# Performance work log

Measured on AMD Instinct MI355X. Metric: run time of the kernel, lower is better.

The kernel has to match this reference:

```python
import jax, jax.numpy as jnp
import numpy as np

N_U = 50000
N_I = 50000
E = 800000
E_LBL = 200000
D_IN = 128
HID = 256
OUT = 128


def setup_inputs() -> dict:
    key = jax.random.key(0)
    ks = jax.random.split(key, 32)
    def glorot(k, shp):
        fan = shp[0] + shp[1]
        return jax.random.uniform(k, shp, jnp.float32, -1.0, 1.0) * np.sqrt(6.0 / fan)
    inp = {
        'x_user': jax.random.normal(ks[0], (N_U, D_IN), jnp.float32),
        'x_item': jax.random.normal(ks[1], (N_I, D_IN), jnp.float32),
        'edge_ui': jax.random.randint(ks[2], (2, E), 0, N_U, jnp.int32),
        'edge_iu': jax.random.randint(ks[3], (2, E), 0, N_I, jnp.int32),
        'edge_lbl': jax.random.randint(ks[4], (2, E_LBL), 0, N_U, jnp.int32),
        # layer 0 SAGE params (src_dim=D_IN, dst_dim=D_IN)
        'w_msg_ui0': glorot(ks[5], (D_IN, HID)), 'b_ui0': jnp.zeros((HID,), jnp.float32), 'w_root_ui0': glorot(ks[6], (D_IN, HID)),
        'w_msg_iu0': glorot(ks[7], (D_IN, HID)), 'b_iu0': jnp.zeros((HID,), jnp.float32), 'w_root_iu0': glorot(ks[8], (D_IN, HID)),
        # layer 1 SAGE params (src_dim=HID, dst_dim=HID)
        'w_msg_ui1': glorot(ks[9], (HID, HID)), 'b_ui1': jnp.zeros((HID,), jnp.float32), 'w_root_ui1': glorot(ks[10], (HID, HID)),
        'w_msg_iu1': glorot(ks[11], (HID, HID)), 'b_iu1': jnp.zeros((HID,), jnp.float32), 'w_root_iu1': glorot(ks[12], (HID, HID)),
        # per-node-type output linears on JK concat (2*HID -> OUT)
        'w_lin_u': glorot(ks[13], (2 * HID, OUT)), 'b_lin_u': jnp.zeros((OUT,), jnp.float32),
        'w_lin_i': glorot(ks[14], (2 * HID, OUT)), 'b_lin_i': jnp.zeros((OUT,), jnp.float32),
    }
    return inp


def _sage(x_src, x_dst, edge, w_msg, b_msg, w_root):
    # PyG SAGEConv(aggr='mean'): lin_l(mean_{j in N(i)} x_src[j]) + lin_r(x_dst[i])
    src, dst = edge[0], edge[1]
    n_dst = x_dst.shape[0]
    agg = jax.ops.segment_sum(x_src[src], dst, num_segments=n_dst)          # [n_dst, d_src]
    cnt = jax.ops.segment_sum(jnp.ones((edge.shape[1],), x_src.dtype), dst, num_segments=n_dst)
    mean = agg / jnp.maximum(cnt, 1.0)[:, None]
    return mean @ w_msg + b_msg + x_dst @ w_root


def reference(x_user, x_item, edge_ui, edge_iu, edge_lbl,
              w_msg_ui0, b_ui0, w_root_ui0, w_msg_iu0, b_iu0, w_root_iu0,
              w_msg_ui1, b_ui1, w_root_ui1, w_msg_iu1, b_iu1, w_root_iu1,
              w_lin_u, b_lin_u, w_lin_i, b_lin_i):
    # ----- encode: 2 HeteroConv(SAGEConv) layers -----
    item0 = _sage(x_user, x_item, edge_ui, w_msg_ui0, b_ui0, w_root_ui0)    # user->item
    user0 = _sage(x_item, x_user, edge_iu, b_msg=b_iu0, w_msg=w_msg_iu0, x_src=None, x_dst=None, edge=None, w_root=None) if False else _sage(x_item, x_user, edge_iu, w_msg_iu0, b_iu0, w_root_iu0)  # item->user
    item1 = _sage(user0, item0, edge_ui, w_msg_ui1, b_ui1, w_root_ui1)
    user1 = _sage(item0, user0, edge_iu, w_msg_iu1, b_iu1, w_root_iu1)
    # ----- JumpingKnowledge 'cat' + per-node-type linear -----
    z_user = jnp.concatenate([user0, user1], axis=-1) @ w_lin_u + b_lin_u   # [N_U, OUT]
    z_item = jnp.concatenate([item0, item1], axis=-1) @ w_lin_i + b_lin_i   # [N_I, OUT]
    # ----- decode: dot product over candidate edges (user, buys, item) -----
    pred = jnp.sum(z_user[edge_lbl[0]] * z_item[edge_lbl[1]], axis=-1)      # [E_LBL]
    return pred
```

## Files before the change

### kernel.cpp

```cpp
#include <hip/hip_runtime.h>

#define NU 50000
#define NI 50000
#define NE 800000
#define NLBL 200000
#define DIN 128
#define HID 256
#define DOUT 128

#define NSLICE 128
#define SLICE_SZ 6250
#define HALF_N 25000

typedef unsigned short ushort_t;
typedef __attribute__((ext_vector_type(8))) short bf16x8;
typedef __attribute__((ext_vector_type(4))) float f32x4;

__device__ __forceinline__ float bf2f(unsigned int u_shifted) {
    union { unsigned int i; float f; } v;
    v.i = u_shifted;
    return v.f;
}
__device__ __forceinline__ float bf_lo(unsigned int u) { return bf2f(u << 16); }
__device__ __forceinline__ float bf_hi(unsigned int u) { return bf2f(u & 0xffff0000u); }
__device__ __forceinline__ ushort_t f2bf(float f) {
    union { float f; unsigned int i; } v;
    v.f = f;
    unsigned int r = (v.i + 0x7FFFu + ((v.i >> 16) & 1u)) >> 16;
    return (ushort_t)r;
}
__device__ __forceinline__ void load_lds16(const ushort_t* g, ushort_t* s) {
    __builtin_amdgcn_global_load_lds(
        (const __attribute__((address_space(1))) void*)g,
        (__attribute__((address_space(3))) void*)s, 16, 0, 0);
}

#define CVT_PER 782
#define CVT_B (2 * CVT_PER)
#define SA_B 512
#define HIST_B (2 * NSLICE * 2)

struct P1Args {
    const int *eui, *eiu;
    ushort_t* cnt_s;
    const float *wm_ui1, *wr_ui1, *wm_iu1, *wr_iu1, *lin_i, *lin_u;
    float *G_i, *S_i, *G_u, *S_u;
    int* scan_part;
    const float* xu; ushort_t* xbu; const float* xi; ushort_t* xbi;
};

__global__ __launch_bounds__(256) void phase1(P1Args a) {
    __shared__ unsigned int cnt[HALF_N / 2];
    int b = blockIdx.x, t = threadIdx.x;
    if (b < HIST_B) {
        int g = b >> 8, s = (b >> 1) & 127, half = b & 1;
        for (int i = t; i < HALF_N / 2; i += 256) cnt[i] = 0;
        __syncthreads();
        const int* dst = (g ? a.eiu : a.eui) + NE;
        int hbase = half * HALF_N;
        int e0 = s * SLICE_SZ;
        for (int i = e0 + t; i < e0 + SLICE_SZ; i += 256) {
            int d = dst[i] - hbase;
            if ((unsigned)d < (unsigned)HALF_N)
                atomicAdd(&cnt[d >> 1], 1u << ((d & 1) * 16));
        }
        __syncthreads();
        unsigned int* outp = (unsigned int*)(a.cnt_s + ((size_t)(g * NSLICE + s)) * 50000 + hbase);
        for (int i = t; i < HALF_N / 2; i += 256) outp[i] = cnt[i];
    } else if (b < HIST_B + SA_B) {
        int r2 = b - HIST_B;
        int which = r2 >> 7;
        int e = (r2 & 127) * 256 + t;
        int k = e >> 7, n = e & 127;
        const float* W = (which == 0) ? a.wm_ui1 : (which == 1) ? a.wr_ui1
                       : (which == 2) ? a.wm_iu1 : a.wr_iu1;
        const float* L = (which < 2) ? a.lin_i : a.lin_u;
        float* O = (which == 0) ? a.G_i : (which == 1) ? a.S_i
                 : (which == 2) ? a.G_u : a.S_u;
        float s = (which & 1) ? L[k * 128 + n] : 0.f;
#pragma unroll 4
        for (int j = 0; j < HID; ++j) s += W[k * HID + j] * L[(HID + j) * 128 + n];
        O[k * 128 + n] = s;
    } else if (b == HIST_B + SA_B) {
        if (t < 64) a.scan_part[t] = 0;
    } else {
        int cb = b - (HIST_B + SA_B + 1);
        int which = (cb >= CVT_PER);
        if (which) cb -= CVT_PER;
        const float4* in = (const float4*)(which ? a.xi : a.xu);
        uint2* outp = (uint2*)(which ? a.xbi : a.xbu);
        const int n4 = NU * DIN / 4;
#pragma unroll
        for (int k = 0; k < 8; ++k) {
            int i = cb * 2048 + k * 256 + t;
            if (i < n4) {
                float4 v = in[i];
                uint2 o;
                o.x = (unsigned int)f2bf(v.x) | ((unsigned int)f2bf(v.y) << 16);
                o.y = (unsigned int)f2bf(v.z) | ((unsigned int)f2bf(v.w) << 16);
                outp[i] = o;
            }
        }
    }
}

struct SscanP2Args {
    ushort_t* cnt_s;
    int* totals;
    int* scan_part;
    const float *wm_ui0, *wr_ui0, *wm_iu0, *wr_iu0;
    const float *G_i, *S_i, *G_u, *S_u;
    const float *b_ui0, *b_iu0, *b_ui1, *b_iu1, *lin_i, *lin_u, *bl_i, *bl_u;
    ushort_t *VT1_i, *VT2_i, *VT3_i, *VT1_u, *VT2_u, *VT3_u;
    float *bz_i, *bz_u;
};

__global__ __launch_bounds__(256) void sscan_prep2(SscanP2Args a) {
    __shared__ int wsum[4];
    int b = blockIdx.x, t = threadIdx.x;
    if (b < 392) {
        if (b == 0 && t == 0) a.totals[100000] = 2 * NE;
        int idx = b * 256 + t;
        int run = 0;
        if (idx < 100000) {
            int g = idx / 50000, node = idx - g * 50000;
            size_t base = (size_t)g * NSLICE * 50000 + node;
#pragma unroll 4
            for (int s = 0; s < NSLICE; ++s) {
                size_t o = base + (size_t)s * 50000;
                int c = a.cnt_s[o];
                a.cnt_s[o] = (ushort_t)run;
                run += c;
            }
            a.totals[idx] = run;
        }
        int s = run;
#pragma unroll
        for (int off = 32; off > 0; off >>= 1) s += __shfl_down(s, off, 64);
        if ((t & 63) == 0) wsum[t >> 6] = s;
        __syncthreads();
        if (t == 0) atomicAdd(&a.scan_part[b >> 3], wsum[0] + wsum[1] + wsum[2] + wsum[3]);
    } else {
        int task = b - 392;
        if (task < 384) {
            int v = task >> 6;
            int e = (task & 63) * 256 + t;
            int k = e >> 7, n = e & 127;
            const float *A1, *X1, *A2 = nullptr, *X2 = nullptr;
            ushort_t* O;
            switch (v) {
                case 0: A1 = a.wm_ui0; X1 = a.S_i; A2 = a.wr_iu0; X2 = a.G_i; O = a.VT1_i; break;
                case 1: A1 = a.wr_ui0; X1 = a.S_i; O = a.VT2_i; break;
                case 2: A1 = a.wm_iu0; X1 = a.G_i; O = a.VT3_i; break;
                case 3: A1 = a.wm_iu0; X1 = a.S_u; A2 = a.wr_ui0; X2 = a.G_u; O = a.VT1_u; break;
                case 4: A1 = a.wr_iu0; X1 = a.S_u; O = a.VT2_u; break;
                default: A1 = a.wm_ui0; X1 = a.G_u; O = a.VT3_u; break;
            }
            float s = 0.f;
#pragma unroll 4
            for (int j = 0; j < HID; ++j) s += A1[k * HID + j] * X1[j * 128 + n];
            if (A2) {
#pragma unroll 4
                for (int j = 0; j < HID; ++j) s += A2[k * HID + j] * X2[j * 128 + n];
            }
            O[n * 128 + k] = f2bf(s);
        } else if (t < 128) {
            int user = task - 384;
            int n = t;
            const float* S = user ? a.S_u : a.S_i;
            const float* G = user ? a.G_u : a.G_i;
            const float* b_own0 = user ? a.b_iu0 : a.b_ui0;
            const float* b_oth0 = user ? a.b_ui0 : a.b_iu0;
            const float* b_own1 = user ? a.b_iu1 : a.b_ui1;
            const float* lin = user ? a.lin_u : a.lin_i;
            const float* bl = user ? a.bl_u : a.bl_i;
            float* o = user ? a.bz_u : a.bz_i;
            float s = bl[n];
            for (int j = 0; j < HID; ++j)
                s += b_own0[j] * S[j * 128 + n] + b_oth0[j] * G[j * 128 + n] +
                     b_own1[j] * lin[(HID + j) * 128 + n];
            o[n] = s;
        }
    }
}

__global__ __launch_bounds__(256) void scan3(int* __restrict__ d, const int* __restrict__ part,
                                             int n, int nb) {
    __shared__ int wsum[4];
    __shared__ int blockoff_sh;
    int b = blockIdx.x, t = threadIdx.x;
    int lane = t & 63, wv = t >> 6;
    if (t < 64) {
        int v = (t < nb) ? part[t] : 0;
        int incl = v;
#pragma unroll
        for (int off = 1; off < 64; off <<= 1) {
            int tv = __shfl_up(incl, off, 64);
            if (t >= off) incl += tv;
        }
        if (t == b) blockoff_sh = incl - v;
    }
    int i0 = b * 2048 + t * 8;
    int v[8];
    int tsum = 0;
#pragma unroll
    for (int k = 0; k < 8; ++k) {
        v[k] = (i0 + k < n) ? d[i0 + k] : 0;
        tsum += v[k];
    }
    int incl = tsum;
#pragma unroll
    for (int off = 1; off < 64; off <<= 1) {
        int tv = __shfl_up(incl, off, 64);
        if (lane >= off) incl += tv;
    }
    if (lane == 63) wsum[wv] = incl;
    __syncthreads();
    int woff = 0;
    for (int w = 0; w < wv; ++w) woff += wsum[w];
    int run = blockoff_sh + woff + (incl - tsum);
#pragma unroll
    for (int k = 0; k < 8; ++k) {
        if (i0 + k < n) d[i0 + k] = run;
        run += v[k];
    }
}

__global__ __launch_bounds__(256) void fill_lds(const int* __restrict__ eui,
                                                const int* __restrict__ eiu,
                                                const ushort_t* __restrict__ cnt_s,
                                                const int* __restrict__ rowstart,
                                                ushort_t* __restrict__ csr) {
    __shared__ unsigned int off[HALF_N / 2];
    int b = blockIdx.x, t = threadIdx.x;
    int g = b >> 8, s = (b >> 1) & 127, half = b & 1;
    const unsigned int* st =
        (const unsigned int*)(cnt_s + ((size_t)(g * NSLICE + s)) * 50000 + half * HALF_N);
    for (int i = t; i < HALF_N / 2; i += 256) off[i] = st[i];
    __syncthreads();
    const int* src = g ? eiu : eui;
    const int* dst = src + NE;
    const int* rs = rowstart + g * 50000;
    int hbase = half * HALF_N;
    int e0 = s * SLICE_SZ;
    for (int i = e0 + t; i < e0 + SLICE_SZ; i += 256) {
        int dd = dst[i];
        int d = dd - hbase;
        if ((unsigned)d < (unsigned)HALF_N) {
            unsigned old = atomicAdd(&off[d >> 1], 1u << ((d & 1) * 16));
            int rel = (int)((old >> ((d & 1) * 16)) & 0xffffu);
            csr[(size_t)rs[dd] + rel] = (ushort_t)src[i];
        }
    }
}

struct AggJob { const int* sp; const ushort_t* csr; const ushort_t* x; ushort_t* out; int n; };
struct AggJobs2 { AggJob j[2]; };

__global__ __launch_bounds__(256) void agg_din(AggJobs2 js) {
    AggJob jb = js.j[blockIdx.y];
    const int half = blockIdx.z;
    int wave = (int)((blockIdx.x * 256u + threadIdx.x) >> 6);
    int lane = threadIdx.x & 63;
    const int l = lane & 15;
    const int h = lane >> 4;
    int w4 = wave * 4;
    if (w4 >= jb.n) return;
    int w = w4 + h;
    int s0 = jb.sp[w];
    int s1 = jb.sp[w + 1];
    int cnt = s1 - s0;
    float sc = (cnt > 0) ? 1.0f / (float)cnt : 0.0f;
    int cmax = cnt;
    {
        int c1 = __shfl_xor(cmax, 16, 64); cmax = (cmax > c1) ? cmax : c1;
        int c2 = __shfl_xor(cmax, 32, 64); cmax = (cmax > c2) ? cmax : c2;
    }
    const uint2* xp = (const uint2*)jb.x + half * 16;
    float f0 = 0.f, f1 = 0.f, f2 = 0.f, f3 = 0.f;
#define ACC4(m, u)                                                     \
    f0 = fmaf(m, bf_lo(u.x), f0); f1 = fmaf(m, bf_hi(u.x), f1);        \
    f2 = fmaf(m, bf_lo(u.y), f2); f3 = fmaf(m, bf_hi(u.y), f3);
    for (int chunk = 0; chunk < cmax; chunk += 16) {
        int mh = cnt - chunk;
        int safe = (mh > 0) ? ((l < mh) ? l : mh - 1) : 0;
        int vidx = (int)jb.csr[s0 + chunk + safe];
        int mm = cmax - chunk;
        if (mm > 16) mm = 16;
        int j = 0;
        for (; j + 3 < mm; j += 4) {
            int i0 = __shfl(vidx, j, 16);
            int i1 = __shfl(vidx, j + 1, 16);
            int i2 = __shfl(vidx, j + 2, 16);
            int i3 = __shfl(vidx, j + 3, 16);
            float m0 = (j < mh) ? 1.f : 0.f;
            float m1 = (j + 1 < mh) ? 1.f : 0.f;
            float m2 = (j + 2 < mh) ? 1.f : 0.f;
            float m3 = (j + 3 < mh) ? 1.f : 0.f;
            uint2 u0 = xp[(size_t)((j < mh) ? i0 : 0) * 32 + l];
            uint2 u1 = xp[(size_t)((j + 1 < mh) ? i1 : 0) * 32 + l];
            uint2 u2 = xp[(size_t)((j + 2 < mh) ? i2 : 0) * 32 + l];
            uint2 u3 = xp[(size_t)((j + 3 < mh) ? i3 : 0) * 32 + l];
            ACC4(m0, u0);
            ACC4(m1, u1);
            ACC4(m2, u2);
            ACC4(m3, u3);
        }
        for (; j < mm; ++j) {
            int i0 = __shfl(vidx, j, 16);
            float m0 = (j < mh) ? 1.f : 0.f;
            uint2 u0 = xp[(size_t)((j < mh) ? i0 : 0) * 32 + l];
            ACC4(m0, u0);
        }
    }
#undef ACC4
    uint2 o;
    o.x = (unsigned int)f2bf(f0 * sc) | ((unsigned int)f2bf(f1 * sc) << 16);
    o.y = (unsigned int)f2bf(f2 * sc) | ((unsigned int)f2bf(f3 * sc) << 16);
    ((uint2*)jb.out)[(size_t)w * 32 + half * 16 + l] = o;
}

struct GemmJob {
    const ushort_t* A[3];
    const ushort_t* WT[3];
    int K[3];
    const float* bias;
    void* C;
};
struct GemmJobs2 { GemmJob j[2]; };

template <int NP, typename OutT>
__global__ __launch_bounds__(256) void gemmN(GemmJobs2 js, int M, int N) {
    GemmJob jb = js.j[blockIdx.z];
    __shared__ ushort_t sA[128 * 32];
    __shared__ ushort_t sB[128 * 32];
    const int tid = threadIdx.x;
    const int lane = tid & 63;
    const int wv = tid >> 6;
    const int wm = wv & 1, wn = wv >> 1;
    const int bm = blockIdx.y * 128, bn = blockIdx.x * 128;

    f32x4 acc[4][4] = {};

    const int srow = tid >> 2;
    const int scol = (tid & 3) * 8;

#pragma unroll
    for (int part = 0; part < NP; ++part) {
        const ushort_t* A = jb.A[part];
        const ushort_t* WT = jb.WT[part];
        const int K = jb.K[part];
        int ar0 = bm + srow;       if (ar0 > M - 1) ar0 = M - 1;
        int ar1 = bm + 64 + srow;  if (ar1 > M - 1) ar1 = M - 1;
        const size_t aoff0 = (size_t)ar0 * K + scol;
        const size_t aoff1 = (size_t)ar1 * K + scol;
        const size_t boff0 = (size_t)(bn + srow) * K + scol;
        const size_t boff1 = (size_t)(bn + 64 + srow) * K + scol;
        for (int k0 = 0; k0 < K; k0 += 32) {
            __syncthreads();
            load_lds16(A + aoff0 + k0, sA + tid * 8);
            load_lds16(A + aoff1 + k0, sA + 2048 + tid * 8);
            load_lds16(WT + boff0 + k0, sB + tid * 8);
            load_lds16(WT + boff1 + k0, sB + 2048 + tid * 8);
            __syncthreads();
            const ushort_t* pA = sA + ((wm * 64 + (lane & 15)) * 32 + (lane >> 4) * 8);
            const ushort_t* pB = sB + ((wn * 64 + (lane & 15)) * 32 + (lane >> 4) * 8);
            bf16x8 af[4], bfr[4];
#pragma unroll
            for (int mt = 0; mt < 4; ++mt) af[mt] = *(const bf16x8*)(pA + mt * 512);
#pragma unroll
            for (int nt = 0; nt < 4; ++nt) bfr[nt] = *(const bf16x8*)(pB + nt * 512);
#pragma unroll
            for (int mt = 0; mt < 4; ++mt)
#pragma unroll
                for (int nt = 0; nt < 4; ++nt)
                    acc[mt][nt] = __builtin_amdgcn_mfma_f32_16x16x32_bf16(
                        af[mt], bfr[nt], acc[mt][nt], 0, 0, 0);
        }
    }

#pragma unroll
    for (int mt = 0; mt < 4; ++mt) {
#pragma unroll
        for (int r = 0; r < 4; ++r) {
            int row = bm + wm * 64 + mt * 16 + (lane >> 4) * 4 + r;
            if (row >= M) continue;
#pragma unroll
            for (int nt = 0; nt < 4; ++nt) {
                int col = bn + wn * 64 + nt * 16 + (lane & 15);
                float v = acc[mt][nt][r] + jb.bias[col];
                if constexpr (sizeof(OutT) == 2)
                    ((ushort_t*)jb.C)[(size_t)row * N + col] = f2bf(v);
                else
                    ((float*)jb.C)[(size_t)row * N + col] = v;
            }
        }
    }
}

__global__ void decode_kernel(const int* __restrict__ lbl, const ushort_t* __restrict__ zu,
                              const ushort_t* __restrict__ zi, float* __restrict__ out, int n) {
    int gid = blockIdx.x * blockDim.x + threadIdx.x;
    int wave = gid >> 6;
    int lane = threadIdx.x & 63;
    int q = lane >> 4;
    int l = lane & 15;
    int e = wave * 4 + q;
    if (e >= n) return;
    int u = lbl[e];
    int it = lbl[n + e];
    uint4 a = ((const uint4*)zu)[(size_t)u * 16 + l];
    uint4 b = ((const uint4*)zi)[(size_t)it * 16 + l];
    float s = bf_lo(a.x) * bf_lo(b.x) + bf_hi(a.x) * bf_hi(b.x) +
              bf_lo(a.y) * bf_lo(b.y) + bf_hi(a.y) * bf_hi(b.y) +
              bf_lo(a.z) * bf_lo(b.z) + bf_hi(a.z) * bf_hi(b.z) +
              bf_lo(a.w) * bf_lo(b.w) + bf_hi(a.w) * bf_hi(b.w);
#pragma unroll
    for (int off = 8; off > 0; off >>= 1) s += __shfl_down(s, off, 16);
    if (l == 0) out[e] = s;
}

extern "C" void kernel_launch(void* const* d_in, const int* in_sizes, int n_in,
                              void* d_out, int out_size, void* d_ws, size_t ws_size,
                              hipStream_t stream) {
    const float* x_user = (const float*)d_in[0];
    const float* x_item = (const float*)d_in[1];
    const int* edge_ui = (const int*)d_in[2];
    const int* edge_iu = (const int*)d_in[3];
    const int* edge_lbl = (const int*)d_in[4];
    const float* w_msg_ui0 = (const float*)d_in[5];
    const float* b_ui0 = (const float*)d_in[6];
    const float* w_root_ui0 = (const float*)d_in[7];
    const float* w_msg_iu0 = (const float*)d_in[8];
    const float* b_iu0 = (const float*)d_in[9];
    const float* w_root_iu0 = (const float*)d_in[10];
    const float* w_msg_ui1 = (const float*)d_in[11];
    const float* b_ui1 = (const float*)d_in[12];
    const float* w_root_ui1 = (const float*)d_in[13];
    const float* w_msg_iu1 = (const float*)d_in[14];
    const float* b_iu1 = (const float*)d_in[15];
    const float* w_root_iu1 = (const float*)d_in[16];
    const float* w_lin_u = (const float*)d_in[17];
    const float* b_lin_u = (const float*)d_in[18];
    const float* w_lin_i = (const float*)d_in[19];
    const float* b_lin_i = (const float*)d_in[20];
    float* out = (float*)d_out;

    char* p = (char*)d_ws;
    ushort_t* A_i  = (ushort_t*)p;   p += (size_t)NI * DIN * 2;
    ushort_t* A_u  = (ushort_t*)p;   p += (size_t)NU * DIN * 2;
    ushort_t* B_i  = (ushort_t*)p;   p += (size_t)NI * DIN * 2;
    ushort_t* B_u  = (ushort_t*)p;   p += (size_t)NU * DIN * 2;
    ushort_t* xb_u  = (ushort_t*)p;  p += (size_t)NU * DIN * 2;
    ushort_t* xb_i  = (ushort_t*)p;  p += (size_t)NI * DIN * 2;
    ushort_t* z_user = (ushort_t*)p; p += (size_t)NU * DOUT * 2;
    ushort_t* z_item = (ushort_t*)p; p += (size_t)NI * DOUT * 2;
    int* totals     = (int*)p;       p += (size_t)(100000 + 64) * 4;
    ushort_t* csr   = (ushort_t*)p;  p += (size_t)2 * NE * 2;
    ushort_t* cnt_s = (ushort_t*)p;  p += (size_t)2 * NSLICE * 50000 * 2;
    int* scan_part  = (int*)p;       p += 64 * 4;
    float* G_i = (float*)p; p += (size_t)HID * 128 * 4;
    float* S_i = (float*)p; p += (size_t)HID * 128 * 4;
    float* G_u = (float*)p; p += (size_t)HID * 128 * 4;
    float* S_u = (float*)p; p += (size_t)HID * 128 * 4;
    ushort_t* VT1_i = (ushort_t*)p; p += (size_t)128 * 128 * 2;
    ushort_t* VT2_i = (ushort_t*)p; p += (size_t)128 * 128 * 2;
    ushort_t* VT3_i = (ushort_t*)p; p += (size_t)128 * 128 * 2;
    ushort_t* VT1_u = (ushort_t*)p; p += (size_t)128 * 128 * 2;
    ushort_t* VT2_u = (ushort_t*)p; p += (size_t)128 * 128 * 2;
    ushort_t* VT3_u = (ushort_t*)p; p += (size_t)128 * 128 * 2;
    float* bz_i = (float*)p; p += 128 * 4;
    float* bz_u = (float*)p; p += 128 * 4;

    const int NCNT = 100000;
    const int NB = (NCNT + 2047) / 2048;

    P1Args p1;
    p1.eui = edge_ui; p1.eiu = edge_iu; p1.cnt_s = cnt_s;
    p1.wm_ui1 = w_msg_ui1; p1.wr_ui1 = w_root_ui1;
    p1.wm_iu1 = w_msg_iu1; p1.wr_iu1 = w_root_iu1;
    p1.lin_i = w_lin_i; p1.lin_u = w_lin_u;
    p1.G_i = G_i; p1.S_i = S_i; p1.G_u = G_u; p1.S_u = S_u;
    p1.scan_part = scan_part;
    p1.xu = x_user; p1.xbu = xb_u; p1.xi = x_item; p1.xbi = xb_i;
    phase1<<<HIST_B + SA_B + 1 + CVT_B, 256, 0, stream>>>(p1);

    SscanP2Args sp;
    sp.cnt_s = cnt_s; sp.totals = totals; sp.scan_part = scan_part;
    sp.wm_ui0 = w_msg_ui0; sp.wr_ui0 = w_root_ui0;
    sp.wm_iu0 = w_msg_iu0; sp.wr_iu0 = w_root_iu0;
    sp.G_i = G_i; sp.S_i = S_i; sp.G_u = G_u; sp.S_u = S_u;
    sp.b_ui0 = b_ui0; sp.b_iu0 = b_iu0; sp.b_ui1 = b_ui1; sp.b_iu1 = b_iu1;
    sp.lin_i = w_lin_i; sp.lin_u = w_lin_u; sp.bl_i = b_lin_i; sp.bl_u = b_lin_u;
    sp.VT1_i = VT1_i; sp.VT2_i = VT2_i; sp.VT3_i = VT3_i;
    sp.VT1_u = VT1_u; sp.VT2_u = VT2_u; sp.VT3_u = VT3_u;
    sp.bz_i = bz_i; sp.bz_u = bz_u;
    sscan_prep2<<<392 + 386, 256, 0, stream>>>(sp);

    scan3<<<NB, 256, 0, stream>>>(totals, scan_part, NCNT, NB);

    fill_lds<<<HIST_B, 256, 0, stream>>>(edge_ui, edge_iu, cnt_s, totals, csr);

    {
        AggJobs2 aj = {{{totals, csr, xb_u, A_i, NI},
                        {totals + 50000, csr, xb_i, A_u, NU}}};
        agg_din<<<dim3(3125, 2, 2), 256, 0, stream>>>(aj);
    }
    {
        AggJobs2 aj = {{{totals, csr, A_u, B_i, NI},
                        {totals + 50000, csr, A_i, B_u, NU}}};
        agg_din<<<dim3(3125, 2, 2), 256, 0, stream>>>(aj);
    }

    {
        GemmJobs2 gj = {{{{A_i, xb_i, B_i}, {VT1_i, VT2_i, VT3_i}, {DIN, DIN, DIN}, bz_i, z_item},
                         {{A_u, xb_u, B_u}, {VT1_u, VT2_u, VT3_u}, {DIN, DIN, DIN}, bz_u, z_user}}};
        gemmN<3, ushort_t><<<dim3(DOUT / 128, (NU + 127) / 128, 2), 256, 0, stream>>>(gj, NU, DOUT);
    }

    decode_kernel<<<(((NLBL + 3) / 4) * 64 + 255) / 256, 256, 0, stream>>>(
        edge_lbl, z_user, z_item, out, NLBL);
}
```

Baseline: 366.3 us.

## Replace sliced LDS histogram CSR build with global-atomic counting and fill

The CSR construction no longer uses per-slice LDS histograms stored in a large cnt_s buffer. Degrees are now counted with global atomics into totals, scanned directly, and edges are scattered into CSR slots through a global atomic cursor. This removes the 128-slice count matrix and its sequential per-node scan, trading it for contended global atomics and a nondeterministic order of neighbours within each row. A memset is added to zero the counters.

```diff
diff --git a/kernel.cpp b/kernel.cpp
--- a/kernel.cpp
+++ b/kernel.cpp
@@ -8,10 +8,6 @@
 #define HID 256
 #define DOUT 128
 
-#define NSLICE 128
-#define SLICE_SZ 6250
-#define HALF_N 25000
-
 typedef unsigned short ushort_t;
 typedef __attribute__((ext_vector_type(8))) short bf16x8;
 typedef __attribute__((ext_vector_type(4))) float f32x4;
@@ -38,37 +34,38 @@
 #define CVT_PER 782
 #define CVT_B (2 * CVT_PER)
 #define SA_B 512
-#define HIST_B (2 * NSLICE * 2)
+#define HISTA_B 512
 
 struct P1Args {
-    const int *eui, *eiu;
-    ushort_t* cnt_s;
+    const float* xu; ushort_t* xbu; const float* xi; ushort_t* xbi;
     const float *wm_ui1, *wr_ui1, *wm_iu1, *wr_iu1, *lin_i, *lin_u;
     float *G_i, *S_i, *G_u, *S_u;
-    int* scan_part;
-    const float* xu; ushort_t* xbu; const float* xi; ushort_t* xbi;
+    const int *eui, *eiu;
+    int* cnt;
 };
 
 __global__ __launch_bounds__(256) void phase1(P1Args a) {
-    __shared__ unsigned int cnt[HALF_N / 2];
-    int b = blockIdx.x, t = threadIdx.x;
-    if (b < HIST_B) {
-        int g = b >> 8, s = (b >> 1) & 127, half = b & 1;
-        for (int i = t; i < HALF_N / 2; i += 256) cnt[i] = 0;
-        __syncthreads();
-        const int* dst = (g ? a.eiu : a.eui) + NE;
-        int hbase = half * HALF_N;
-        int e0 = s * SLICE_SZ;
-        for (int i = e0 + t; i < e0 + SLICE_SZ; i += 256) {
-            int d = dst[i] - hbase;
-            if ((unsigned)d < (unsigned)HALF_N)
-                atomicAdd(&cnt[d >> 1], 1u << ((d & 1) * 16));
-        }
-        __syncthreads();
-        unsigned int* outp = (unsigned int*)(a.cnt_s + ((size_t)(g * NSLICE + s)) * 50000 + hbase);
-        for (int i = t; i < HALF_N / 2; i += 256) outp[i] = cnt[i];
-    } else if (b < HIST_B + SA_B) {
-        int r2 = b - HIST_B;
+    int b = blockIdx.x;
+    int t = threadIdx.x;
+    if (b < CVT_B) {
+        int which = (b >= CVT_PER);
+        int cb = which ? b - CVT_PER : b;
+        const float4* in = (const float4*)(which ? a.xi : a.xu);
+        uint2* outp = (uint2*)(which ? a.xbi : a.xbu);
+        const int n4 = NU * DIN / 4;
+#pragma unroll
+        for (int k = 0; k < 8; ++k) {
+            int i = cb * 2048 + k * 256 + t;
+            if (i < n4) {
+                float4 v = in[i];
+                uint2 o;
+                o.x = (unsigned int)f2bf(v.x) | ((unsigned int)f2bf(v.y) << 16);
+                o.y = (unsigned int)f2bf(v.z) | ((unsigned int)f2bf(v.w) << 16);
+                outp[i] = o;
+            }
+        }
+    } else if (b < CVT_B + SA_B) {
+        int r2 = b - CVT_B;
         int which = r2 >> 7;
         int e = (r2 & 127) * 256 + t;
         int k = e >> 7, n = e & 127;
@@ -81,32 +78,22 @@
 #pragma unroll 4
         for (int j = 0; j < HID; ++j) s += W[k * HID + j] * L[(HID + j) * 128 + n];
         O[k * 128 + n] = s;
-    } else if (b == HIST_B + SA_B) {
-        if (t < 64) a.scan_part[t] = 0;
     } else {
-        int cb = b - (HIST_B + SA_B + 1);
-        int which = (cb >= CVT_PER);
-        if (which) cb -= CVT_PER;
-        const float4* in = (const float4*)(which ? a.xi : a.xu);
-        uint2* outp = (uint2*)(which ? a.xbi : a.xbu);
-        const int n4 = NU * DIN / 4;
-#pragma unroll
-        for (int k = 0; k < 8; ++k) {
-            int i = cb * 2048 + k * 256 + t;
-            if (i < n4) {
-                float4 v = in[i];
-                uint2 o;
-                o.x = (unsigned int)f2bf(v.x) | ((unsigned int)f2bf(v.y) << 16);
-                o.y = (unsigned int)f2bf(v.z) | ((unsigned int)f2bf(v.w) << 16);
-                outp[i] = o;
-            }
-        }
-    }
-}
-
-struct SscanP2Args {
-    ushort_t* cnt_s;
-    int* totals;
+        int idx = (b - CVT_B - SA_B) * 256 + t;
+        const int stride = HISTA_B * 256;
+        const int* dui = a.eui + NE;
+        const int* diu = a.eiu + NE;
+        for (int i = idx; i < 2 * NE; i += stride) {
+            int g = (i >= NE);
+            int e = i - (g ? NE : 0);
+            int dd = (g ? diu : dui)[e];
+            atomicAdd(&a.cnt[g * 50000 + dd], 1);
+        }
+    }
+}
+
+struct K2Args {
+    const int* totals;
     int* scan_part;
     const float *wm_ui0, *wr_ui0, *wm_iu0, *wr_iu0;
     const float *G_i, *S_i, *G_u, *S_u;
@@ -115,33 +102,21 @@
     float *bz_i, *bz_u;
 };
 
-__global__ __launch_bounds__(256) void sscan_prep2(SscanP2Args a) {
+__global__ __launch_bounds__(256) void k2_scan_prep(K2Args a) {
     __shared__ int wsum[4];
     int b = blockIdx.x, t = threadIdx.x;
-    if (b < 392) {
-        if (b == 0 && t == 0) a.totals[100000] = 2 * NE;
-        int idx = b * 256 + t;
-        int run = 0;
-        if (idx < 100000) {
-            int g = idx / 50000, node = idx - g * 50000;
-            size_t base = (size_t)g * NSLICE * 50000 + node;
-#pragma unroll 4
-            for (int s = 0; s < NSLICE; ++s) {
-                size_t o = base + (size_t)s * 50000;
-                int c = a.cnt_s[o];
-                a.cnt_s[o] = (ushort_t)run;
-                run += c;
-            }
-            a.totals[idx] = run;
-        }
-        int s = run;
+    if (b < 49) {
+        int i0 = b * 2048 + t * 8;
+        int s = 0;
+#pragma unroll
+        for (int k = 0; k < 8; ++k) s += (i0 + k < 100000) ? a.totals[i0 + k] : 0;
 #pragma unroll
         for (int off = 32; off > 0; off >>= 1) s += __shfl_down(s, off, 64);
         if ((t & 63) == 0) wsum[t >> 6] = s;
         __syncthreads();
-        if (t == 0) atomicAdd(&a.scan_part[b >> 3], wsum[0] + wsum[1] + wsum[2] + wsum[3]);
+        if (t == 0) a.scan_part[b] = wsum[0] + wsum[1] + wsum[2] + wsum[3];
     } else {
-        int task = b - 392;
+        int task = b - 49;
         if (task < 384) {
             int v = task >> 6;
             int e = (task & 63) * 256 + t;
@@ -185,11 +160,12 @@
 }
 
 __global__ __launch_bounds__(256) void scan3(int* __restrict__ d, const int* __restrict__ part,
-                                             int n, int nb) {
+                                             int* __restrict__ cursor, int n, int nb) {
     __shared__ int wsum[4];
     __shared__ int blockoff_sh;
     int b = blockIdx.x, t = threadIdx.x;
     int lane = t & 63, wv = t >> 6;
+    if (b == 0 && t == 0) { d[100000] = 2 * NE; cursor[100000] = 2 * NE; }
     if (t < 64) {
         int v = (t < nb) ? part[t] : 0;
         int incl = v;
@@ -221,36 +197,24 @@
     int run = blockoff_sh + woff + (incl - tsum);
 #pragma unroll
     for (int k = 0; k < 8; ++k) {
-        if (i0 + k < n) d[i0 + k] = run;
+        if (i0 + k < n) { d[i0 + k] = run; cursor[i0 + k] = run; }
         run += v[k];
     }
 }
 
-__global__ __launch_bounds__(256) void fill_lds(const int* __restrict__ eui,
-                                                const int* __restrict__ eiu,
-                                                const ushort_t* __restrict__ cnt_s,
-                                                const int* __restrict__ rowstart,
-                                                ushort_t* __restrict__ csr) {
-    __shared__ unsigned int off[HALF_N / 2];
-    int b = blockIdx.x, t = threadIdx.x;
-    int g = b >> 8, s = (b >> 1) & 127, half = b & 1;
-    const unsigned int* st =
-        (const unsigned int*)(cnt_s + ((size_t)(g * NSLICE + s)) * 50000 + half * HALF_N);
-    for (int i = t; i < HALF_N / 2; i += 256) off[i] = st[i];
-    __syncthreads();
-    const int* src = g ? eiu : eui;
-    const int* dst = src + NE;
-    const int* rs = rowstart + g * 50000;
-    int hbase = half * HALF_N;
-    int e0 = s * SLICE_SZ;
-    for (int i = e0 + t; i < e0 + SLICE_SZ; i += 256) {
-        int dd = dst[i];
-        int d = dd - hbase;
-        if ((unsigned)d < (unsigned)HALF_N) {
-            unsigned old = atomicAdd(&off[d >> 1], 1u << ((d & 1) * 16));
-            int rel = (int)((old >> ((d & 1) * 16)) & 0xffffu);
-            csr[(size_t)rs[dd] + rel] = (ushort_t)src[i];
-        }
+__global__ __launch_bounds__(256) void fill_atomic(const int* __restrict__ eui,
+                                                   const int* __restrict__ eiu,
+                                                   int* __restrict__ cursor,
+                                                   ushort_t* __restrict__ csr) {
+    int idx = blockIdx.x * 256 + threadIdx.x;
+    const int stride = (int)(gridDim.x * 256);
+    for (int i = idx; i < 2 * NE; i += stride) {
+        int g = (i >= NE);
+        int e = i - (g ? NE : 0);
+        const int* src = g ? eiu : eui;
+        int dd = src[NE + e];
+        int pos = atomicAdd(&cursor[g * 50000 + dd], 1);
+        csr[pos] = (ushort_t)src[e];
     }
 }
 
@@ -456,8 +420,8 @@
     ushort_t* z_user = (ushort_t*)p; p += (size_t)NU * DOUT * 2;
     ushort_t* z_item = (ushort_t*)p; p += (size_t)NI * DOUT * 2;
     int* totals     = (int*)p;       p += (size_t)(100000 + 64) * 4;
+    int* cursor     = (int*)p;       p += (size_t)(100000 + 64) * 4;
     ushort_t* csr   = (ushort_t*)p;  p += (size_t)2 * NE * 2;
-    ushort_t* cnt_s = (ushort_t*)p;  p += (size_t)2 * NSLICE * 50000 * 2;
     int* scan_part  = (int*)p;       p += 64 * 4;
     float* G_i = (float*)p; p += (size_t)HID * 128 * 4;
     float* S_i = (float*)p; p += (size_t)HID * 128 * 4;
@@ -475,31 +439,33 @@
     const int NCNT = 100000;
     const int NB = (NCNT + 2047) / 2048;
 
+    hipMemsetAsync(totals, 0, (size_t)(NCNT + 1) * 4, stream);
+
     P1Args p1;
-    p1.eui = edge_ui; p1.eiu = edge_iu; p1.cnt_s = cnt_s;
+    p1.xu = x_user; p1.xbu = xb_u; p1.xi = x_item; p1.xbi = xb_i;
     p1.wm_ui1 = w_msg_ui1; p1.wr_ui1 = w_root_ui1;
     p1.wm_iu1 = w_msg_iu1; p1.wr_iu1 = w_root_iu1;
     p1.lin_i = w_lin_i; p1.lin_u = w_lin_u;
     p1.G_i = G_i; p1.S_i = S_i; p1.G_u = G_u; p1.S_u = S_u;
-    p1.scan_part = scan_part;
-    p1.xu = x_user; p1.xbu = xb_u; p1.xi = x_item; p1.xbi = xb_i;
-    phase1<<<HIST_B + SA_B + 1 + CVT_B, 256, 0, stream>>>(p1);
-
-    SscanP2Args sp;
-    sp.cnt_s = cnt_s; sp.totals = totals; sp.scan_part = scan_part;
-    sp.wm_ui0 = w_msg_ui0; sp.wr_ui0 = w_root_ui0;
-    sp.wm_iu0 = w_msg_iu0; sp.wr_iu0 = w_root_iu0;
-    sp.G_i = G_i; sp.S_i = S_i; sp.G_u = G_u; sp.S_u = S_u;
-    sp.b_ui0 = b_ui0; sp.b_iu0 = b_iu0; sp.b_ui1 = b_ui1; sp.b_iu1 = b_iu1;
-    sp.lin_i = w_lin_i; sp.lin_u = w_lin_u; sp.bl_i = b_lin_i; sp.bl_u = b_lin_u;
-    sp.VT1_i = VT1_i; sp.VT2_i = VT2_i; sp.VT3_i = VT3_i;
-    sp.VT1_u = VT1_u; sp.VT2_u = VT2_u; sp.VT3_u = VT3_u;
-    sp.bz_i = bz_i; sp.bz_u = bz_u;
-    sscan_prep2<<<392 + 386, 256, 0, stream>>>(sp);
-
-    scan3<<<NB, 256, 0, stream>>>(totals, scan_part, NCNT, NB);
-
-    fill_lds<<<HIST_B, 256, 0, stream>>>(edge_ui, edge_iu, cnt_s, totals, csr);
+    p1.eui = edge_ui; p1.eiu = edge_iu;
+    p1.cnt = totals;
+    phase1<<<CVT_B + SA_B + HISTA_B, 256, 0, stream>>>(p1);
+
+    K2Args k2;
+    k2.totals = totals; k2.scan_part = scan_part;
+    k2.wm_ui0 = w_msg_ui0; k2.wr_ui0 = w_root_ui0;
+    k2.wm_iu0 = w_msg_iu0; k2.wr_iu0 = w_root_iu0;
+    k2.G_i = G_i; k2.S_i = S_i; k2.G_u = G_u; k2.S_u = S_u;
+    k2.b_ui0 = b_ui0; k2.b_iu0 = b_iu0; k2.b_ui1 = b_ui1; k2.b_iu1 = b_iu1;
+    k2.lin_i = w_lin_i; k2.lin_u = w_lin_u; k2.bl_i = b_lin_i; k2.bl_u = b_lin_u;
+    k2.VT1_i = VT1_i; k2.VT2_i = VT2_i; k2.VT3_i = VT3_i;
+    k2.VT1_u = VT1_u; k2.VT2_u = VT2_u; k2.VT3_u = VT3_u;
+    k2.bz_i = bz_i; k2.bz_u = bz_u;
+    k2_scan_prep<<<49 + 386, 256, 0, stream>>>(k2);
+
+    scan3<<<NB, 256, 0, stream>>>(totals, scan_part, cursor, NCNT, NB);
+
+    fill_atomic<<<2048, 256, 0, stream>>>(edge_ui, edge_iu, cursor, csr);
 
     {
         AggJobs2 aj = {{{totals, csr, xb_u, A_i, NI},
```

New measurement: 469.8 us. 28.3% more time.

## Split histogram/fill into quarter-range blocks and move bf16 conversion to second kernel

Applied to the files above, without the earlier changes.

The histogram and CSR fill kernels now split each edge slice's destination range into four quarters instead of two. This halves the per-block LDS footprint so more blocks can be resident, at the cost of each block scanning its edge slice with more blocks overall. The fp32-to-bf16 feature conversion blocks move from phase1 into the scan/prep kernel. That rebalances work across the two launches and shortens the first, histogram-bound kernel.

```diff
diff --git a/kernel.cpp b/kernel.cpp
--- a/kernel.cpp
+++ b/kernel.cpp
@@ -10,7 +10,8 @@
 
 #define NSLICE 128
 #define SLICE_SZ 6250
-#define HALF_N 25000
+#define QN 12500
+#define NQ 4
 
 typedef unsigned short ushort_t;
 typedef __attribute__((ext_vector_type(8))) short bf16x8;
@@ -38,7 +39,7 @@
 #define CVT_PER 782
 #define CVT_B (2 * CVT_PER)
 #define SA_B 512
-#define HIST_B (2 * NSLICE * 2)
+#define HIST_B (2 * NSLICE * NQ)
 
 struct P1Args {
     const int *eui, *eiu;
@@ -46,27 +47,26 @@
     const float *wm_ui1, *wr_ui1, *wm_iu1, *wr_iu1, *lin_i, *lin_u;
     float *G_i, *S_i, *G_u, *S_u;
     int* scan_part;
-    const float* xu; ushort_t* xbu; const float* xi; ushort_t* xbi;
 };
 
 __global__ __launch_bounds__(256) void phase1(P1Args a) {
-    __shared__ unsigned int cnt[HALF_N / 2];
+    __shared__ unsigned int cnt[QN / 2];
     int b = blockIdx.x, t = threadIdx.x;
     if (b < HIST_B) {
-        int g = b >> 8, s = (b >> 1) & 127, half = b & 1;
-        for (int i = t; i < HALF_N / 2; i += 256) cnt[i] = 0;
+        int g = b >> 9, s = (b >> 2) & 127, q = b & 3;
+        for (int i = t; i < QN / 2; i += 256) cnt[i] = 0;
         __syncthreads();
         const int* dst = (g ? a.eiu : a.eui) + NE;
-        int hbase = half * HALF_N;
+        int hbase = q * QN;
         int e0 = s * SLICE_SZ;
         for (int i = e0 + t; i < e0 + SLICE_SZ; i += 256) {
             int d = dst[i] - hbase;
-            if ((unsigned)d < (unsigned)HALF_N)
+            if ((unsigned)d < (unsigned)QN)
                 atomicAdd(&cnt[d >> 1], 1u << ((d & 1) * 16));
         }
         __syncthreads();
         unsigned int* outp = (unsigned int*)(a.cnt_s + ((size_t)(g * NSLICE + s)) * 50000 + hbase);
-        for (int i = t; i < HALF_N / 2; i += 256) outp[i] = cnt[i];
+        for (int i = t; i < QN / 2; i += 256) outp[i] = cnt[i];
     } else if (b < HIST_B + SA_B) {
         int r2 = b - HIST_B;
         int which = r2 >> 7;
@@ -81,30 +81,12 @@
 #pragma unroll 4
         for (int j = 0; j < HID; ++j) s += W[k * HID + j] * L[(HID + j) * 128 + n];
         O[k * 128 + n] = s;
-    } else if (b == HIST_B + SA_B) {
+    } else {
         if (t < 64) a.scan_part[t] = 0;
-    } else {
-        int cb = b - (HIST_B + SA_B + 1);
-        int which = (cb >= CVT_PER);
-        if (which) cb -= CVT_PER;
-        const float4* in = (const float4*)(which ? a.xi : a.xu);
-        uint2* outp = (uint2*)(which ? a.xbi : a.xbu);
-        const int n4 = NU * DIN / 4;
-#pragma unroll
-        for (int k = 0; k < 8; ++k) {
-            int i = cb * 2048 + k * 256 + t;
-            if (i < n4) {
-                float4 v = in[i];
-                uint2 o;
-                o.x = (unsigned int)f2bf(v.x) | ((unsigned int)f2bf(v.y) << 16);
-                o.y = (unsigned int)f2bf(v.z) | ((unsigned int)f2bf(v.w) << 16);
-                outp[i] = o;
-            }
-        }
-    }
-}
-
-struct SscanP2Args {
+    }
+}
+
+struct K2Args {
     ushort_t* cnt_s;
     int* totals;
     int* scan_part;
@@ -113,9 +95,10 @@
     const float *b_ui0, *b_iu0, *b_ui1, *b_iu1, *lin_i, *lin_u, *bl_i, *bl_u;
     ushort_t *VT1_i, *VT2_i, *VT3_i, *VT1_u, *VT2_u, *VT3_u;
     float *bz_i, *bz_u;
+    const float* xu; ushort_t* xbu; const float* xi; ushort_t* xbi;
 };
 
-__global__ __launch_bounds__(256) void sscan_prep2(SscanP2Args a) {
+__global__ __launch_bounds__(256) void k2_scan_prep_cvt(K2Args a) {
     __shared__ int wsum[4];
     int b = blockIdx.x, t = threadIdx.x;
     if (b < 392) {
@@ -140,7 +123,7 @@
         if ((t & 63) == 0) wsum[t >> 6] = s;
         __syncthreads();
         if (t == 0) atomicAdd(&a.scan_part[b >> 3], wsum[0] + wsum[1] + wsum[2] + wsum[3]);
-    } else {
+    } else if (b < 778) {
         int task = b - 392;
         if (task < 384) {
             int v = task >> 6;
@@ -181,6 +164,24 @@
                      b_own1[j] * lin[(HID + j) * 128 + n];
             o[n] = s;
         }
+    } else {
+        int cb = b - 778;
+        int which = (cb >= CVT_PER);
+        if (which) cb -= CVT_PER;
+        const float4* in = (const float4*)(which ? a.xi : a.xu);
+        uint2* outp = (uint2*)(which ? a.xbi : a.xbu);
+        const int n4 = NU * DIN / 4;
+#pragma unroll
+        for (int k = 0; k < 8; ++k) {
+            int i = cb * 2048 + k * 256 + t;
+            if (i < n4) {
+                float4 v = in[i];
+                uint2 o;
+                o.x = (unsigned int)f2bf(v.x) | ((unsigned int)f2bf(v.y) << 16);
+                o.y = (unsigned int)f2bf(v.z) | ((unsigned int)f2bf(v.w) << 16);
+                outp[i] = o;
+            }
+        }
     }
 }
 
@@ -231,22 +232,22 @@
                                                 const ushort_t* __restrict__ cnt_s,
                                                 const int* __restrict__ rowstart,
                                                 ushort_t* __restrict__ csr) {
-    __shared__ unsigned int off[HALF_N / 2];
+    __shared__ unsigned int off[QN / 2];
     int b = blockIdx.x, t = threadIdx.x;
-    int g = b >> 8, s = (b >> 1) & 127, half = b & 1;
+    int g = b >> 9, s = (b >> 2) & 127, q = b & 3;
+    int hbase = q * QN;
     const unsigned int* st =
-        (const unsigned int*)(cnt_s + ((size_t)(g * NSLICE + s)) * 50000 + half * HALF_N);
-    for (int i = t; i < HALF_N / 2; i += 256) off[i] = st[i];
+        (const unsigned int*)(cnt_s + ((size_t)(g * NSLICE + s)) * 50000 + hbase);
+    for (int i = t; i < QN / 2; i += 256) off[i] = st[i];
     __syncthreads();
     const int* src = g ? eiu : eui;
     const int* dst = src + NE;
     const int* rs = rowstart + g * 50000;
-    int hbase = half * HALF_N;
     int e0 = s * SLICE_SZ;
     for (int i = e0 + t; i < e0 + SLICE_SZ; i += 256) {
         int dd = dst[i];
         int d = dd - hbase;
-        if ((unsigned)d < (unsigned)HALF_N) {
+        if ((unsigned)d < (unsigned)QN) {
             unsigned old = atomicAdd(&off[d >> 1], 1u << ((d & 1) * 16));
             int rel = (int)((old >> ((d & 1) * 16)) & 0xffffu);
             csr[(size_t)rs[dd] + rel] = (ushort_t)src[i];
@@ -482,20 +483,20 @@
     p1.lin_i = w_lin_i; p1.lin_u = w_lin_u;
     p1.G_i = G_i; p1.S_i = S_i; p1.G_u = G_u; p1.S_u = S_u;
     p1.scan_part = scan_part;
-    p1.xu = x_user; p1.xbu = xb_u; p1.xi = x_item; p1.xbi = xb_i;
-    phase1<<<HIST_B + SA_B + 1 + CVT_B, 256, 0, stream>>>(p1);
-
-    SscanP2Args sp;
-    sp.cnt_s = cnt_s; sp.totals = totals; sp.scan_part = scan_part;
-    sp.wm_ui0 = w_msg_ui0; sp.wr_ui0 = w_root_ui0;
-    sp.wm_iu0 = w_msg_iu0; sp.wr_iu0 = w_root_iu0;
-    sp.G_i = G_i; sp.S_i = S_i; sp.G_u = G_u; sp.S_u = S_u;
-    sp.b_ui0 = b_ui0; sp.b_iu0 = b_iu0; sp.b_ui1 = b_ui1; sp.b_iu1 = b_iu1;
-    sp.lin_i = w_lin_i; sp.lin_u = w_lin_u; sp.bl_i = b_lin_i; sp.bl_u = b_lin_u;
-    sp.VT1_i = VT1_i; sp.VT2_i = VT2_i; sp.VT3_i = VT3_i;
-    sp.VT1_u = VT1_u; sp.VT2_u = VT2_u; sp.VT3_u = VT3_u;
-    sp.bz_i = bz_i; sp.bz_u = bz_u;
-    sscan_prep2<<<392 + 386, 256, 0, stream>>>(sp);
+    phase1<<<HIST_B + SA_B + 1, 256, 0, stream>>>(p1);
+
+    K2Args k2;
+    k2.cnt_s = cnt_s; k2.totals = totals; k2.scan_part = scan_part;
+    k2.wm_ui0 = w_msg_ui0; k2.wr_ui0 = w_root_ui0;
+    k2.wm_iu0 = w_msg_iu0; k2.wr_iu0 = w_root_iu0;
+    k2.G_i = G_i; k2.S_i = S_i; k2.G_u = G_u; k2.S_u = S_u;
+    k2.b_ui0 = b_ui0; k2.b_iu0 = b_iu0; k2.b_ui1 = b_ui1; k2.b_iu1 = b_iu1;
+    k2.lin_i = w_lin_i; k2.lin_u = w_lin_u; k2.bl_i = b_lin_i; k2.bl_u = b_lin_u;
+    k2.VT1_i = VT1_i; k2.VT2_i = VT2_i; k2.VT3_i = VT3_i;
+    k2.VT1_u = VT1_u; k2.VT2_u = VT2_u; k2.VT3_u = VT3_u;
+    k2.bz_i = bz_i; k2.bz_u = bz_u;
+    k2.xu = x_user; k2.xbu = xb_u; k2.xi = x_item; k2.xbi = xb_i;
+    k2_scan_prep_cvt<<<392 + 386 + CVT_B, 256, 0, stream>>>(k2);
 
     scan3<<<NB, 256, 0, stream>>>(totals, scan_part, NCNT, NB);
 
```

After: 356.8 us. 1.03x faster.
